# Kernel optimization log

Hardware: AMD Instinct MI355X
Metric: run time of the kernel (lower is better)

The kernel has to match this reference:

```python
import jax, jax.numpy as jnp
import numpy as np

SIZE = 768

def setup_inputs() -> dict:
    key = jax.random.key(0)
    k = jax.random.split(key, 8)
    bs, A_len, P_len, l = 16, 1024, 2048, SIZE
    s = 1.0 / np.sqrt(l)
    A = jax.random.normal(k[0], (bs, A_len, l), dtype=jnp.float32)
    P = jax.random.normal(k[1], (bs, P_len, l), dtype=jnp.float32)
    G_w = jax.random.normal(k[2], (l, l), dtype=jnp.float32) * s
    G_b = jax.random.normal(k[3], (l,), dtype=jnp.float32) * 0.01
    fca_w = jax.random.normal(k[4], (2 * l, l), dtype=jnp.float32) * (1.0 / np.sqrt(2 * l))
    fca_b = jax.random.normal(k[5], (l,), dtype=jnp.float32) * 0.01
    fcp_w = jax.random.normal(k[6], (2 * l, l), dtype=jnp.float32) * (1.0 / np.sqrt(2 * l))
    fcp_b = jax.random.normal(k[7], (l,), dtype=jnp.float32) * 0.01
    return {"A": A, "P": P, "G_w": G_w, "G_b": G_b,
            "fca_w": fca_w, "fca_b": fca_b, "fcp_w": fcp_w, "fcp_b": fcp_b}


def reference(A, P, G_w, G_b, fca_w, fca_b, fcp_w, fcp_b):
    # Ag: projected answer states [b, a, l]
    Ag = jnp.einsum('bal,lm->bam', A, G_w) + G_b
    # scores [b, p, a]; softmax over A_len (last dim), as in torch (dim=-1)
    W = jnp.einsum('bpl,bal->bpa', P, Ag)
    W = jax.nn.softmax(W, axis=-1)
    # MP: [b, p, l] attend over A; MA: [b, a, l] = W^T @ P (unnormalized over p)
    MP = jnp.einsum('bpa,bal->bpl', W, Ag)
    MA = jnp.einsum('bpa,bpl->bal', W, P)
    SA = jnp.concatenate([MA - Ag, MA * Ag], axis=2)  # [b, a, 2l]
    SP = jnp.concatenate([MP - P, MP * P], axis=2)    # [b, p, 2l]
    SA = jax.nn.relu(jnp.einsum('bak,kl->bal', SA, fca_w) + fca_b)
    SP = jax.nn.relu(jnp.einsum('bpk,kl->bpl', SP, fcp_w) + fcp_b)
    return (SA, SP)
```

## Files before the change

kernel.cpp:

```cpp
#include <hip/hip_runtime.h>

typedef _Float16 h8 __attribute__((ext_vector_type(8)));
typedef _Float16 h4 __attribute__((ext_vector_type(4)));
typedef float    f4 __attribute__((ext_vector_type(4)));

__global__ __launch_bounds__(256)
void conv_f16(const float* __restrict__ in, _Float16* __restrict__ out)
{
    size_t i = ((size_t)blockIdx.x * 256 + threadIdx.x) * 8;
    float4 a = *(const float4*)(in + i);
    float4 b = *(const float4*)(in + i + 4);
    h8 o;
    o[0] = (_Float16)a.x; o[1] = (_Float16)a.y; o[2] = (_Float16)a.z; o[3] = (_Float16)a.w;
    o[4] = (_Float16)b.x; o[5] = (_Float16)b.y; o[6] = (_Float16)b.z; o[7] = (_Float16)b.w;
    *(h8*)(out + i) = o;
}

template<int F32IN>
__global__ __launch_bounds__(256)
void transpose_conv(const void* __restrict__ inv, _Float16* __restrict__ out,
                    int R, int C, long sIn, long sOut)
{
    __shared__ _Float16 tile[32][33];
    const int z = blockIdx.z;
    const int c0 = blockIdx.x * 32, r0 = blockIdx.y * 32;
    const int tx = threadIdx.x & 31, ty = threadIdx.x >> 5;
    if constexpr (F32IN) {
        const float* in = (const float*)inv + (size_t)z * sIn;
        #pragma unroll
        for (int i = 0; i < 4; ++i)
            tile[ty + 8 * i][tx] = (_Float16)in[(size_t)(r0 + ty + 8 * i) * C + c0 + tx];
    } else {
        const _Float16* in = (const _Float16*)inv + (size_t)z * sIn;
        #pragma unroll
        for (int i = 0; i < 4; ++i)
            tile[ty + 8 * i][tx] = in[(size_t)(r0 + ty + 8 * i) * C + c0 + tx];
    }
    __syncthreads();
    out += (size_t)z * sOut;
    #pragma unroll
    for (int i = 0; i < 4; ++i)
        out[(size_t)(c0 + ty + 8 * i) * R + r0 + tx] = tile[tx][ty + 8 * i];
}

__global__ __launch_bounds__(256)
void softmax1024(const float* __restrict__ S, _Float16* __restrict__ W)
{
    __shared__ float red[256];
    const int t = threadIdx.x;
    const float* p = S + (size_t)blockIdx.x * 1024;

    float v[4];
    *(float4*)v = ((const float4*)p)[t];

    float m = fmaxf(fmaxf(v[0], v[1]), fmaxf(v[2], v[3]));
    red[t] = m;
    __syncthreads();
    for (int s = 128; s > 0; s >>= 1) {
        if (t < s) red[t] = fmaxf(red[t], red[t + s]);
        __syncthreads();
    }
    m = red[0];
    __syncthreads();

    float sum = 0.f;
    #pragma unroll
    for (int j = 0; j < 4; ++j) { v[j] = __expf(v[j] - m); sum += v[j]; }
    red[t] = sum;
    __syncthreads();
    for (int s = 128; s > 0; s >>= 1) {
        if (t < s) red[t] += red[t + s];
        __syncthreads();
    }
    const float inv = 1.0f / red[0];

    h4 o;
    #pragma unroll
    for (int j = 0; j < 4; ++j) o[j] = (_Float16)(v[j] * inv);
    *(h4*)(W + (size_t)blockIdx.x * 1024 + t * 4) = o;
}

template<int CONCAT, int BIAS, int RELU, int OUT>
__global__ __launch_bounds__(256)
void gemm_mfma(const _Float16* __restrict__ A0, const _Float16* __restrict__ A1,
               const _Float16* __restrict__ B, const float* __restrict__ bias,
               void* __restrict__ Cv, _Float16* __restrict__ CT,
               int K, int lda, int ldb, int ldc,
               long sA, long sB, long sC,
               int mtbShift, long sCT)
{
    __shared__ _Float16 As[128][40];
    __shared__ _Float16 Bs[128][40];

    const int t = threadIdx.x;
    const int z = blockIdx.z;
    A0 += (size_t)z * sA;
    if constexpr (CONCAT) A1 += (size_t)z * sA;
    B  += (size_t)z * sB;

    const int m0 = blockIdx.y * 128, n0 = blockIdx.x * 128;
    const int wave = t >> 6, lane = t & 63, quad = lane >> 4, lcol = lane & 15;
    const int wm = (wave >> 1) * 64, wn = (wave & 1) * 64;

    const int arow = t >> 2;
    const int akg  = (t & 3) * 8;

    f4 acc[4][4] = {};

    for (int k0 = 0; k0 < K; k0 += 32) {
        #pragma unroll
        for (int h = 0; h < 2; ++h) {
            const int row = arow + h * 64;
            if constexpr (!CONCAT) {
                h8 v = *(const h8*)(A0 + (size_t)(m0 + row) * lda + k0 + akg);
                *(h8*)&As[row][akg] = v;
            } else {
                const int kk = k0 + akg;
                const bool hi = kk >= lda;
                const int kb = hi ? kk - lda : kk;
                h8 x = *(const h8*)(A0 + (size_t)(m0 + row) * lda + kb);
                h8 y = *(const h8*)(A1 + (size_t)(m0 + row) * lda + kb);
                h8 r;
                #pragma unroll
                for (int j = 0; j < 8; ++j)
                    r[j] = hi ? (_Float16)(x[j] * y[j]) : (_Float16)(x[j] - y[j]);
                *(h8*)&As[row][akg] = r;
            }
            h8 w = *(const h8*)(B + (size_t)(n0 + row) * ldb + k0 + akg);
            *(h8*)&Bs[row][akg] = w;
        }
        __syncthreads();

        h8 af[4], bg[4];
        #pragma unroll
        for (int i = 0; i < 4; ++i) {
            af[i] = *(const h8*)&As[wm + i * 16 + lcol][quad * 8];
            bg[i] = *(const h8*)&Bs[wn + i * 16 + lcol][quad * 8];
        }
        #pragma unroll
        for (int i = 0; i < 4; ++i)
            #pragma unroll
            for (int j = 0; j < 4; ++j)
                acc[i][j] = __builtin_amdgcn_mfma_f32_16x16x32_f16(af[i], bg[j], acc[i][j], 0, 0, 0);
        __syncthreads();
    }

    #pragma unroll
    for (int mi = 0; mi < 4; ++mi) {
        #pragma unroll
        for (int nj = 0; nj < 4; ++nj) {
            const int gm = m0 + wm + mi * 16 + quad * 4;
            const int gn = n0 + wn + nj * 16 + lcol;
            float bv = 0.f;
            if constexpr (BIAS) bv = bias[gn];
            if constexpr (OUT == 0) {
                float* C = (float*)Cv + (size_t)z * sC;
                #pragma unroll
                for (int r = 0; r < 4; ++r) {
                    float v = acc[mi][nj][r] + bv;
                    if constexpr (RELU) v = fmaxf(v, 0.f);
                    C[(size_t)(gm + r) * ldc + gn] = v;
                }
            } else {
                _Float16* C = (_Float16*)Cv + (size_t)z * sC;
                _Float16 tmp[4];
                #pragma unroll
                for (int r = 0; r < 4; ++r) {
                    float v = acc[mi][nj][r] + bv;
                    if constexpr (RELU) v = fmaxf(v, 0.f);
                    tmp[r] = (_Float16)v;
                    C[(size_t)(gm + r) * ldc + gn] = tmp[r];
                }
                if constexpr (OUT == 2) {
                    const int zz = gm >> mtbShift;
                    const int ml = gm & ((1 << mtbShift) - 1);
                    h4 o; o[0] = tmp[0]; o[1] = tmp[1]; o[2] = tmp[2]; o[3] = tmp[3];
                    *(h4*)(CT + (size_t)zz * sCT + ((size_t)gn << mtbShift) + ml) = o;
                }
            }
        }
    }
}

extern "C" void kernel_launch(void* const* d_in, const int* in_sizes, int n_in,
                              void* d_out, int out_size, void* d_ws, size_t ws_size,
                              hipStream_t stream)
{
    const float* A     = (const float*)d_in[0];
    const float* P     = (const float*)d_in[1];
    const float* G_w   = (const float*)d_in[2];
    const float* G_b   = (const float*)d_in[3];
    const float* fca_w = (const float*)d_in[4];
    const float* fca_b = (const float*)d_in[5];
    const float* fcp_w = (const float*)d_in[6];
    const float* fcp_b = (const float*)d_in[7];

    const int BS = 16, AL = 1024, PL = 2048, L = 768;

    _Float16* w = (_Float16*)d_ws;
    size_t off = 0;
    _Float16* P_h  = w + off; off += (size_t)BS * PL * L;
    _Float16* PT_h = w + off; off += (size_t)BS * PL * L;
    _Float16* A_h  = w + off; off += (size_t)BS * AL * L;
    _Float16* Ag_h = w + off; off += (size_t)BS * AL * L;
    _Float16* AgT  = w + off; off += (size_t)BS * AL * L;
    _Float16* W_h  = w + off; off += (size_t)BS * PL * AL;
    _Float16* MP_h = w + off; off += (size_t)BS * PL * L;
    _Float16* MA_h = w + off; off += (size_t)BS * AL * L;
    _Float16* GwT  = w + off; off += (size_t)L * L;
    _Float16* fcaT = w + off; off += (size_t)2 * L * L;
    _Float16* fcpT = w + off; off += (size_t)2 * L * L;
    if (ws_size < off * sizeof(_Float16)) return;

    float*    scores = (float*)d_out;
    _Float16* WT_h   = (_Float16*)d_out;
    float*    SA = (float*)d_out;
    float*    SP = SA + (size_t)BS * AL * L;

    conv_f16<<<(BS * AL * L) / (256 * 8), 256, 0, stream>>>(A, A_h);
    conv_f16<<<(BS * PL * L) / (256 * 8), 256, 0, stream>>>(P, P_h);
    transpose_conv<1><<<dim3(L / 32, PL / 32, BS), 256, 0, stream>>>(
        P, PT_h, PL, L, (long)PL * L, (long)PL * L);
    transpose_conv<1><<<dim3(L / 32, L / 32, 1), 256, 0, stream>>>(
        G_w, GwT, L, L, 0, 0);
    transpose_conv<1><<<dim3(L / 32, 2 * L / 32, 1), 256, 0, stream>>>(
        fca_w, fcaT, 2 * L, L, 0, 0);
    transpose_conv<1><<<dim3(L / 32, 2 * L / 32, 1), 256, 0, stream>>>(
        fcp_w, fcpT, 2 * L, L, 0, 0);

    gemm_mfma<0, 1, 0, 2><<<dim3(L / 128, BS * AL / 128, 1), 256, 0, stream>>>(
        A_h, nullptr, GwT, G_b, Ag_h, AgT,
        L, L, L, L, 0, 0, 0, 10, (long)L * AL);

    gemm_mfma<0, 0, 0, 0><<<dim3(AL / 128, PL / 128, BS), 256, 0, stream>>>(
        P_h, nullptr, Ag_h, nullptr, scores, nullptr,
        L, L, L, AL, (long)PL * L, (long)AL * L, (long)PL * AL, 0, 0);

    softmax1024<<<BS * PL, 256, 0, stream>>>(scores, W_h);

    transpose_conv<0><<<dim3(AL / 32, PL / 32, BS), 256, 0, stream>>>(
        W_h, WT_h, PL, AL, (long)PL * AL, (long)PL * AL);

    gemm_mfma<0, 0, 0, 1><<<dim3(L / 128, PL / 128, BS), 256, 0, stream>>>(
        W_h, nullptr, AgT, nullptr, MP_h, nullptr,
        AL, AL, AL, L, (long)PL * AL, (long)L * AL, (long)PL * L, 0, 0);

    gemm_mfma<0, 0, 0, 1><<<dim3(L / 128, AL / 128, BS), 256, 0, stream>>>(
        WT_h, nullptr, PT_h, nullptr, MA_h, nullptr,
        PL, PL, PL, L, (long)AL * PL, (long)L * PL, (long)AL * L, 0, 0);

    gemm_mfma<1, 1, 1, 0><<<dim3(L / 128, BS * AL / 128, 1), 256, 0, stream>>>(
        MA_h, Ag_h, fcaT, fca_b, SA, nullptr,
        2 * L, L, 2 * L, L, 0, 0, 0, 0, 0);

    gemm_mfma<1, 1, 1, 0><<<dim3(L / 128, BS * PL / 128, 1), 256, 0, stream>>>(
        MP_h, P_h, fcpT, fcp_b, SP, nullptr,
        2 * L, L, 2 * L, L, 0, 0, 0, 0, 0);
}
```

Before: 1.069 ms.

## Use direct global-to-LDS loads and wider 128x256 GEMM tiles

Replaces the GEMM kernel with a templated version that stages A and B tiles into shared memory via global_load_lds, bypassing registers, and removes the padded LDS layout. Most GEMMs now use 128x256 output tiles (NF=8), which gives more MFMA reuse per loaded tile. The P transpose is now done from the fp16 copy rather than the fp32 input, halving its read traffic. The unpadded LDS layout may add bank conflicts on fragment reads, and the wider tiles raise register pressure while halving the number of blocks.

New measurement: 931.7 us. 12.8% less time.

```diff
diff --git a/kernel.cpp b/kernel.cpp
--- a/kernel.cpp
+++ b/kernel.cpp
@@ -3,6 +3,12 @@
 typedef _Float16 h8 __attribute__((ext_vector_type(8)));
 typedef _Float16 h4 __attribute__((ext_vector_type(4)));
 typedef float    f4 __attribute__((ext_vector_type(4)));
+
+__device__ __forceinline__ void glds16(const void* g, void* l) {
+    __builtin_amdgcn_global_load_lds(
+        (const __attribute__((address_space(1))) unsigned*)g,
+        (__attribute__((address_space(3))) unsigned*)l, 16, 0, 0);
+}
 
 __global__ __launch_bounds__(256)
 void conv_f16(const float* __restrict__ in, _Float16* __restrict__ out)
@@ -80,67 +86,74 @@
     *(h4*)(W + (size_t)blockIdx.x * 1024 + t * 4) = o;
 }
 
-template<int CONCAT, int BIAS, int RELU, int OUT>
-__global__ __launch_bounds__(256)
-void gemm_mfma(const _Float16* __restrict__ A0, const _Float16* __restrict__ A1,
-               const _Float16* __restrict__ B, const float* __restrict__ bias,
-               void* __restrict__ Cv, _Float16* __restrict__ CT,
-               int K, int lda, int ldb, int ldc,
-               long sA, long sB, long sC,
-               int mtbShift, long sCT)
-{
-    __shared__ _Float16 As[128][40];
-    __shared__ _Float16 Bs[128][40];
+template<int NF, int CONCAT, int BIAS, int RELU, int OUT>
+__global__ __launch_bounds__(256, 2)
+void gemm_k(const _Float16* __restrict__ A0, const _Float16* __restrict__ A1,
+            const _Float16* __restrict__ B, const float* __restrict__ bias,
+            void* __restrict__ Cv, _Float16* __restrict__ CT,
+            int K, int lda, int ldb, int ldc,
+            long sA, long sB, long sC, int mtbShift, long sCT)
+{
+    constexpr int TN = NF * 32;
+    __shared__ _Float16 As[128 * 32];
+    __shared__ _Float16 Bs[TN * 32];
 
     const int t = threadIdx.x;
     const int z = blockIdx.z;
     A0 += (size_t)z * sA;
     if constexpr (CONCAT) A1 += (size_t)z * sA;
-    B  += (size_t)z * sB;
-
-    const int m0 = blockIdx.y * 128, n0 = blockIdx.x * 128;
+    B += (size_t)z * sB;
+
+    const int m0 = blockIdx.y * 128, n0 = blockIdx.x * TN;
     const int wave = t >> 6, lane = t & 63, quad = lane >> 4, lcol = lane & 15;
-    const int wm = (wave >> 1) * 64, wn = (wave & 1) * 64;
-
-    const int arow = t >> 2;
-    const int akg  = (t & 3) * 8;
-
-    f4 acc[4][4] = {};
+    const int wm = (wave >> 1) * 64, wn = (wave & 1) * (NF * 16);
+
+    const int srow = t >> 2;
+    const int scol = (t & 3) * 8;
+    const int wb = wave * 1024;
+
+    f4 acc[4][NF] = {};
 
     for (int k0 = 0; k0 < K; k0 += 32) {
-        #pragma unroll
-        for (int h = 0; h < 2; ++h) {
-            const int row = arow + h * 64;
-            if constexpr (!CONCAT) {
-                h8 v = *(const h8*)(A0 + (size_t)(m0 + row) * lda + k0 + akg);
-                *(h8*)&As[row][akg] = v;
-            } else {
-                const int kk = k0 + akg;
-                const bool hi = kk >= lda;
-                const int kb = hi ? kk - lda : kk;
-                h8 x = *(const h8*)(A0 + (size_t)(m0 + row) * lda + kb);
-                h8 y = *(const h8*)(A1 + (size_t)(m0 + row) * lda + kb);
+        if constexpr (!CONCAT) {
+            #pragma unroll
+            for (int h = 0; h < 2; ++h)
+                glds16(A0 + (size_t)(m0 + srow + h * 64) * lda + k0 + scol,
+                       (char*)As + h * 4096 + wb);
+        } else {
+            const int kk = k0 + scol;
+            const bool hi = kk >= lda;
+            const int kb = hi ? kk - lda : kk;
+            #pragma unroll
+            for (int h = 0; h < 2; ++h) {
+                const size_t rb = (size_t)(m0 + srow + h * 64) * lda + kb;
+                h8 x = *(const h8*)(A0 + rb);
+                h8 y = *(const h8*)(A1 + rb);
                 h8 r;
                 #pragma unroll
                 for (int j = 0; j < 8; ++j)
                     r[j] = hi ? (_Float16)(x[j] * y[j]) : (_Float16)(x[j] - y[j]);
-                *(h8*)&As[row][akg] = r;
+                *(h8*)&As[(srow + h * 64) * 32 + scol] = r;
             }
-            h8 w = *(const h8*)(B + (size_t)(n0 + row) * ldb + k0 + akg);
-            *(h8*)&Bs[row][akg] = w;
         }
-        __syncthreads();
-
-        h8 af[4], bg[4];
-        #pragma unroll
-        for (int i = 0; i < 4; ++i) {
-            af[i] = *(const h8*)&As[wm + i * 16 + lcol][quad * 8];
-            bg[i] = *(const h8*)&Bs[wn + i * 16 + lcol][quad * 8];
-        }
+        #pragma unroll
+        for (int h = 0; h < TN / 64; ++h)
+            glds16(B + (size_t)(n0 + srow + h * 64) * ldb + k0 + scol,
+                   (char*)Bs + h * 4096 + wb);
+
+        __syncthreads();
+
+        h8 af[4], bg[NF];
+        #pragma unroll
+        for (int i = 0; i < 4; ++i)
+            af[i] = *(const h8*)&As[(wm + i * 16 + lcol) * 32 + quad * 8];
+        #pragma unroll
+        for (int j = 0; j < NF; ++j)
+            bg[j] = *(const h8*)&Bs[(wn + j * 16 + lcol) * 32 + quad * 8];
         #pragma unroll
         for (int i = 0; i < 4; ++i)
             #pragma unroll
-            for (int j = 0; j < 4; ++j)
+            for (int j = 0; j < NF; ++j)
                 acc[i][j] = __builtin_amdgcn_mfma_f32_16x16x32_f16(af[i], bg[j], acc[i][j], 0, 0, 0);
         __syncthreads();
     }
@@ -148,7 +161,7 @@
     #pragma unroll
     for (int mi = 0; mi < 4; ++mi) {
         #pragma unroll
-        for (int nj = 0; nj < 4; ++nj) {
+        for (int nj = 0; nj < NF; ++nj) {
             const int gm = m0 + wm + mi * 16 + quad * 4;
             const int gn = n0 + wn + nj * 16 + lcol;
             float bv = 0.f;
@@ -219,20 +232,20 @@
 
     conv_f16<<<(BS * AL * L) / (256 * 8), 256, 0, stream>>>(A, A_h);
     conv_f16<<<(BS * PL * L) / (256 * 8), 256, 0, stream>>>(P, P_h);
-    transpose_conv<1><<<dim3(L / 32, PL / 32, BS), 256, 0, stream>>>(
-        P, PT_h, PL, L, (long)PL * L, (long)PL * L);
     transpose_conv<1><<<dim3(L / 32, L / 32, 1), 256, 0, stream>>>(
         G_w, GwT, L, L, 0, 0);
     transpose_conv<1><<<dim3(L / 32, 2 * L / 32, 1), 256, 0, stream>>>(
         fca_w, fcaT, 2 * L, L, 0, 0);
     transpose_conv<1><<<dim3(L / 32, 2 * L / 32, 1), 256, 0, stream>>>(
         fcp_w, fcpT, 2 * L, L, 0, 0);
-
-    gemm_mfma<0, 1, 0, 2><<<dim3(L / 128, BS * AL / 128, 1), 256, 0, stream>>>(
+    transpose_conv<0><<<dim3(L / 32, PL / 32, BS), 256, 0, stream>>>(
+        P_h, PT_h, PL, L, (long)PL * L, (long)PL * L);
+
+    gemm_k<8, 0, 1, 0, 2><<<dim3(L / 256, BS * AL / 128, 1), 256, 0, stream>>>(
         A_h, nullptr, GwT, G_b, Ag_h, AgT,
         L, L, L, L, 0, 0, 0, 10, (long)L * AL);
 
-    gemm_mfma<0, 0, 0, 0><<<dim3(AL / 128, PL / 128, BS), 256, 0, stream>>>(
+    gemm_k<4, 0, 0, 0, 0><<<dim3(AL / 128, PL / 128, BS), 256, 0, stream>>>(
         P_h, nullptr, Ag_h, nullptr, scores, nullptr,
         L, L, L, AL, (long)PL * L, (long)AL * L, (long)PL * AL, 0, 0);
 
@@ -241,19 +254,19 @@
     transpose_conv<0><<<dim3(AL / 32, PL / 32, BS), 256, 0, stream>>>(
         W_h, WT_h, PL, AL, (long)PL * AL, (long)PL * AL);
 
-    gemm_mfma<0, 0, 0, 1><<<dim3(L / 128, PL / 128, BS), 256, 0, stream>>>(
+    gemm_k<8, 0, 0, 0, 1><<<dim3(L / 256, PL / 128, BS), 256, 0, stream>>>(
         W_h, nullptr, AgT, nullptr, MP_h, nullptr,
         AL, AL, AL, L, (long)PL * AL, (long)L * AL, (long)PL * L, 0, 0);
 
-    gemm_mfma<0, 0, 0, 1><<<dim3(L / 128, AL / 128, BS), 256, 0, stream>>>(
+    gemm_k<8, 0, 0, 0, 1><<<dim3(L / 256, AL / 128, BS), 256, 0, stream>>>(
         WT_h, nullptr, PT_h, nullptr, MA_h, nullptr,
         PL, PL, PL, L, (long)AL * PL, (long)L * PL, (long)AL * L, 0, 0);
 
-    gemm_mfma<1, 1, 1, 0><<<dim3(L / 128, BS * AL / 128, 1), 256, 0, stream>>>(
+    gemm_k<8, 1, 1, 1, 0><<<dim3(L / 256, BS * AL / 128, 1), 256, 0, stream>>>(
         MA_h, Ag_h, fcaT, fca_b, SA, nullptr,
         2 * L, L, 2 * L, L, 0, 0, 0, 0, 0);
 
-    gemm_mfma<1, 1, 1, 0><<<dim3(L / 128, BS * PL / 128, 1), 256, 0, stream>>>(
+    gemm_k<8, 1, 1, 1, 0><<<dim3(L / 256, BS * PL / 128, 1), 256, 0, stream>>>(
         MP_h, P_h, fcpT, fcp_b, SP, nullptr,
         2 * L, L, 2 * L, L, 0, 0, 0, 0, 0);
 }
```
